# Optimization experiments

Measured on AMD Instinct MI355X. Metric: run time of the kernel, lower is better.

Reference implementation:

```python
import jax, jax.numpy as jnp
import numpy as np

B, T, E, H, D = 4, 2048, 1024, 16, 64


def setup_inputs() -> dict:
    key = jax.random.key(0)
    k1, k2, k3, k4 = jax.random.split(key, 4)
    s = 1.0 / np.sqrt(E)
    return {
        "x": jax.random.normal(k1, (B, T, E), dtype=jnp.float32),
        "wj_w": jax.random.uniform(k2, (E, E), jnp.float32, -s, s),   # torch Linear weight (out,in)
        "wjv_w": jax.random.uniform(k3, (E, E), jnp.float32, -s, s),
        "wo_w": jax.random.uniform(k4, (E, H * D), jnp.float32, -s, s),
    }


def reference(x, wj_w, wjv_w, wo_w):
    b, t, e = x.shape
    # echo = x @ wj_w.T ; eb = echo @ wj_w  (F.linear with transposed weight)
    eb = (x @ wj_w.T) @ wj_w
    sc = jnp.sum(x * eb, axis=-1) / jnp.sqrt(jnp.asarray(e, x.dtype))  # (B,T)
    # rank-1 outer-product scores with strict-upper causal mask
    ja = sc[:, :, None] * sc[:, None, :]                               # (B,T,T)
    causal = jnp.tril(jnp.ones((t, t), dtype=bool))
    ja = jnp.where(causal[None], ja, -jnp.inf)
    ja = jax.nn.softmax(ja, axis=-1)                                   # (B,T,T)
    # values per head; attention map shared across heads (broadcast, not materialized)
    val = (x @ wjv_w.T).reshape(b, t, H, D)                            # (B,T,H,D)
    out = jnp.einsum("bts,bshd->bthd", ja, val)                       # (B,T,H,D)
    return out.reshape(b, t, H * D) @ wo_w.T                           # (B,T,E)
```

## Files before the change

kernel.cpp:

```cpp
#include <hip/hip_runtime.h>
#include <math.h>

#define R_ROWS 8192
#define T_SEQ  2048
#define E_DIM  1024
#define KC     32

typedef __attribute__((ext_vector_type(8))) short short8;
typedef __attribute__((ext_vector_type(4))) float f32x4;

__device__ __forceinline__ ushort f2bf(float f) {
  uint u = __float_as_uint(f);
  u += 0x7FFFu + ((u >> 16) & 1u);
  return (ushort)(u >> 16);
}
__device__ __forceinline__ float bf2f(ushort h) {
  return __uint_as_float(((uint)h) << 16);
}


__global__ __launch_bounds__(256) void cvt_split_frag(
    const float* __restrict__ in, ushort* __restrict__ hi,
    ushort* __restrict__ lo, int n)
{
  int g = blockIdx.x * 256 + threadIdx.x;
  if (g >= n) return;
  const int l = g & 15, h = (g >> 4) & 3;
  const int pq = g >> 6;
  const int q = pq & (KC - 1), p = pq >> 5;
  const size_t src = (size_t)(p * 16 + l) * 1024 + q * 32 + h * 8;
  const float4 v0 = *(const float4*)&in[src];
  const float4 v1 = *(const float4*)&in[src + 4];
  ushort hh[8], ll[8];
  const float v[8] = {v0.x, v0.y, v0.z, v0.w, v1.x, v1.y, v1.z, v1.w};
#pragma unroll
  for (int e = 0; e < 8; ++e) {
    hh[e] = f2bf(v[e]);
    ll[e] = f2bf(v[e] - bf2f(hh[e]));
  }
  *(uint4*)&hi[(size_t)g * 8] = *(const uint4*)hh;
  *(uint4*)&lo[(size_t)g * 8] = *(const uint4*)ll;
}

__global__ __launch_bounds__(256) void cvt_bf16_frag(
    const float* __restrict__ in, ushort* __restrict__ out, int n)
{
  int g = blockIdx.x * 256 + threadIdx.x;
  if (g >= n) return;
  const int l = g & 15, h = (g >> 4) & 3;
  const int pq = g >> 6;
  const int q = pq & (KC - 1), p = pq >> 5;
  const size_t src = (size_t)(p * 16 + l) * 1024 + q * 32 + h * 8;
  const float4 v0 = *(const float4*)&in[src];
  const float4 v1 = *(const float4*)&in[src + 4];
  ushort hh[8];
  const float v[8] = {v0.x, v0.y, v0.z, v0.w, v1.x, v1.y, v1.z, v1.w};
#pragma unroll
  for (int e = 0; e < 8; ++e) hh[e] = f2bf(v[e]);
  *(uint4*)&out[(size_t)g * 8] = *(const uint4*)hh;
}

__global__ __launch_bounds__(256) void cvt_bf16(
    const float* __restrict__ in, ushort* __restrict__ out, int n4)
{
  int i = blockIdx.x * 256 + threadIdx.x;
  if (i >= n4) return;
  float4 v = ((const float4*)in)[i];
  ushort4 o;
  o.x = f2bf(v.x); o.y = f2bf(v.y); o.z = f2bf(v.z); o.w = f2bf(v.w);
  ((ushort4*)out)[i] = o;
}

struct Frags { short8 ah[4], al[4], bh[4], bl[4]; };

__global__ __launch_bounds__(256, 2) void gemm_sq_direct(
    const ushort* __restrict__ xh, const ushort* __restrict__ xl,
    const ushort* __restrict__ wh, const ushort* __restrict__ wl,
    float* __restrict__ sc_raw)
{
  const int tid = threadIdx.x;
  const int m0 = blockIdx.y * 128, n0 = blockIdx.x * 128;
  const int wave = tid >> 6, lane = tid & 63;
  const int l15 = lane & 15, lq = lane >> 4;
  const int wm = (wave & 1) * 64, wn = (wave >> 1) * 64;

  size_t aoff[4], boff[4];
#pragma unroll
  for (int i = 0; i < 4; ++i)
    aoff[i] = ((size_t)(((m0 + wm) >> 4) + i) * KC * 4 + lq) * 128 + l15 * 8;
#pragma unroll
  for (int j = 0; j < 4; ++j)
    boff[j] = ((size_t)(((n0 + wn) >> 4) + j) * KC * 4 + lq) * 128 + l15 * 8;

  f32x4 acc[4][4] = {};
  Frags f0, f1;

  auto load = [&](Frags& f, int q) {
    const size_t dq = (size_t)q * 512;
#pragma unroll
    for (int i = 0; i < 4; ++i) {
      f.ah[i] = *(const short8*)(xh + aoff[i] + dq);
      f.al[i] = *(const short8*)(xl + aoff[i] + dq);
    }
#pragma unroll
    for (int j = 0; j < 4; ++j) {
      f.bh[j] = *(const short8*)(wh + boff[j] + dq);
      f.bl[j] = *(const short8*)(wl + boff[j] + dq);
    }
  };
  auto step = [&](const Frags& f) {
#pragma unroll
    for (int i = 0; i < 4; ++i)
#pragma unroll
      for (int j = 0; j < 4; ++j) {
        acc[i][j] = __builtin_amdgcn_mfma_f32_16x16x32_bf16(f.ah[i], f.bh[j], acc[i][j], 0, 0, 0);
        acc[i][j] = __builtin_amdgcn_mfma_f32_16x16x32_bf16(f.ah[i], f.bl[j], acc[i][j], 0, 0, 0);
        acc[i][j] = __builtin_amdgcn_mfma_f32_16x16x32_bf16(f.al[i], f.bh[j], acc[i][j], 0, 0, 0);
      }
  };

  load(f0, 0);
#pragma unroll 1
  for (int q = 0; q < KC; q += 2) {
    load(f1, q + 1);
    step(f0);
    if (q + 2 < KC) load(f0, q + 2);
    step(f1);
  }

  __shared__ float red[128][33];
#pragma unroll
  for (int i = 0; i < 4; ++i)
#pragma unroll
    for (int r = 0; r < 4; ++r) {
      const int row = wm + i * 16 + lq * 4 + r;
      float s = 0.f;
#pragma unroll
      for (int j = 0; j < 4; ++j) s += acc[i][j][r] * acc[i][j][r];
      red[row][(l15 << 1) | (wave >> 1)] = s;
    }
  __syncthreads();
  if (tid < 128) {
    float s = 0.f;
#pragma unroll
    for (int c = 0; c < 32; ++c) s += red[tid][c];
    atomicAdd(&sc_raw[m0 + tid], s);
  }
}

__global__ __launch_bounds__(1024) void scan_max(
    const float* __restrict__ sc_raw, float* __restrict__ sc,
    float* __restrict__ pmax)
{
  const int b = blockIdx.x;
  __shared__ float b0[T_SEQ];
  __shared__ float b1[T_SEQ];
  const int tid = threadIdx.x;
  for (int i = tid; i < T_SEQ; i += 1024) {
    const float v = sc_raw[b*T_SEQ + i] * 0.03125f;
    b0[i] = v;
    sc[b*T_SEQ + i] = v;
  }
  __syncthreads();
  float* src = b0; float* dst = b1;
  for (int off = 1; off < T_SEQ; off <<= 1) {
    for (int i = tid; i < T_SEQ; i += 1024)
      dst[i] = (i >= off) ? fmaxf(src[i], src[i - off]) : src[i];
    __syncthreads();
    float* tmp = src; src = dst; dst = tmp;
  }
  for (int i = tid; i < T_SEQ; i += 1024) pmax[b*T_SEQ + i] = src[i];
}

template<bool OUT_BF16>
__global__ __launch_bounds__(256) void gemm_bf16_bfrag(
    const ushort* __restrict__ A, const ushort* __restrict__ Bf,
    void* __restrict__ Cout, int N, int K)
{
  __shared__ ushort As[128][40];
  const int tid = threadIdx.x;
  const int m0 = blockIdx.y * 128, n0 = blockIdx.x * 128;
  const int wave = tid >> 6, lane = tid & 63;
  const int l15 = lane & 15, lq = lane >> 4;
  const int wm = (wave & 1) * 64, wn = (wave >> 1) * 64;
  const int srow = tid >> 2, scol = (tid & 3) * 8;
  const int Kc = K >> 5;

  f32x4 acc[4][4] = {};
  const ushort* Ap = A + (size_t)(m0 + srow) * K + scol;
  size_t boff[4];
#pragma unroll
  for (int j = 0; j < 4; ++j)
    boff[j] = ((size_t)(((n0 + wn) >> 4) + j) * Kc * 4 + lq) * 128 + l15 * 8;

  for (int q = 0; q < Kc; ++q) {
    const uint4 a0 = *(const uint4*)(Ap + q * 32);
    const uint4 a1 = *(const uint4*)(Ap + (size_t)64 * K + q * 32);
    short8 bfr[4];
#pragma unroll
    for (int j = 0; j < 4; ++j)
      bfr[j] = *(const short8*)(Bf + boff[j] + (size_t)q * 512);
    __syncthreads();
    *(uint4*)&As[srow     ][scol] = a0;
    *(uint4*)&As[srow + 64][scol] = a1;
    __syncthreads();
    short8 af[4];
#pragma unroll
    for (int i = 0; i < 4; ++i)
      af[i] = *(const short8*)&As[wm + i*16 + l15][lq*8];
#pragma unroll
    for (int i = 0; i < 4; ++i)
#pragma unroll
      for (int j = 0; j < 4; ++j)
        acc[i][j] = __builtin_amdgcn_mfma_f32_16x16x32_bf16(af[i], bfr[j], acc[i][j], 0, 0, 0);
  }

#pragma unroll
  for (int i = 0; i < 4; ++i)
#pragma unroll
    for (int j = 0; j < 4; ++j) {
      const int mb = m0 + wm + i*16 + lq*4;
      const int nb = n0 + wn + j*16 + l15;
#pragma unroll
      for (int r = 0; r < 4; ++r) {
        if (OUT_BF16)
          ((ushort*)Cout)[(size_t)(mb + r) * N + nb] = f2bf(acc[i][j][r]);
        else
          ((float*)Cout)[(size_t)(mb + r) * N + nb] = acc[i][j][r];
      }
    }
}

__global__ __launch_bounds__(512) void attn_mfma(
    const ushort* __restrict__ valT, const float* __restrict__ sc,
    const float* __restrict__ pmax, ushort* __restrict__ attnN)
{
  __shared__ float scs_all[T_SEQ];
  __shared__ ushort p[2][128][72];
  __shared__ float zsh[128][4];
  __shared__ float zinv[128];

  const int b  = blockIdx.z;
  const int e0 = blockIdx.x * 128;
  const int tid = threadIdx.x;
  const int wave = tid >> 6, lane = tid & 63;
  const int l15 = lane & 15, lq = lane >> 4;
  const int wm = (wave & 1) * 64;
  const int wn = (wave >> 1) * 32;
  const int bT = b * T_SEQ;

  *(float4*)&scs_all[tid * 4] = *(const float4*)&sc[bT + tid * 4];
  __syncthreads();

  const int prow = tid >> 2;
  const int pc = (tid & 3) * 16;

#pragma unroll 1
  for (int ph = 0; ph < 2; ++ph) {
    const int ty = ph == 0 ? (15 - (int)blockIdx.y) : (int)blockIdx.y;
    const int t0 = ty * 128;
    const int nchunk = 2 * ty + 2;

    const int tglob = t0 + prow;
    const float st = sc[bT + tglob];
    const float pm = pmax[bT + tglob];

    f32x4 acc[4][2] = {};
    float zp = 0.f;

    auto pgen = [&](int c, int buf) -> float {
      const int s0 = c * 64;
      float sv[16];
#pragma unroll
      for (int q = 0; q < 4; ++q)
        *(float4*)&sv[q*4] = *(const float4*)&scs_all[s0 + pc + q*4];
      ushort tmp[16];
      float z = 0.f;
#pragma unroll
      for (int k = 0; k < 16; ++k) {
        const int sg = s0 + pc + k;
        float pe = 0.f;
        if (sg <= tglob) pe = __expf(st * (sv[k] - pm));
        const ushort h = f2bf(pe);
        tmp[k] = h;
        z += bf2f(h);
      }
      *(uint4*)&p[buf][prow][pc    ] = *(const uint4*)&tmp[0];
      *(uint4*)&p[buf][prow][pc + 8] = *(const uint4*)&tmp[8];
      return z;
    };

    auto loadB = [&](short8* dst, int c) {
#pragma unroll
      for (int j = 0; j < 2; ++j)
#pragma unroll
        for (int ksi = 0; ksi < 2; ++ksi)
          dst[j*2 + ksi] = *(const short8*)&valT[
              (size_t)(e0 + wn + j*16 + l15) * R_ROWS + bT + c*64 + ksi*32 + lq*8];
    };

    auto mstep = [&](int buf, const short8* bfr) {
#pragma unroll
      for (int ksi = 0; ksi < 2; ++ksi) {
        short8 af[4];
#pragma unroll
        for (int i = 0; i < 4; ++i)
          af[i] = *(const short8*)&p[buf][wm + i*16 + l15][ksi*32 + lq*8];
#pragma unroll
        for (int i = 0; i < 4; ++i)
#pragma unroll
          for (int j = 0; j < 2; ++j)
            acc[i][j] = __builtin_amdgcn_mfma_f32_16x16x32_bf16(
                af[i], bfr[j*2 + ksi], acc[i][j], 0, 0, 0);
      }
    };

    short8 bA[4], bB[4];
    zp += pgen(0, 0);
    loadB(bA, 0);
    __syncthreads();

#pragma unroll 1
    for (int c = 0; c < nchunk; ++c) {
      if ((c & 1) == 0) {
        if (c + 1 < nchunk) { loadB(bB, c + 1); zp += pgen(c + 1, 1); }
        mstep(0, bA);
      } else {
        if (c + 1 < nchunk) { loadB(bA, c + 1); zp += pgen(c + 1, 0); }
        mstep(1, bB);
      }
      __syncthreads();
    }

    zsh[prow][tid & 3] = zp;
    __syncthreads();
    if (tid < 128)
      zinv[tid] = 1.0f / (zsh[tid][0] + zsh[tid][1] + zsh[tid][2] + zsh[tid][3]);
    __syncthreads();

#pragma unroll
    for (int i = 0; i < 4; ++i)
#pragma unroll
      for (int j = 0; j < 2; ++j) {
        const int nb = e0 + wn + j*16 + l15;
#pragma unroll
        for (int r = 0; r < 4; ++r) {
          const int ml = wm + i*16 + lq*4 + r;
          const float v = acc[i][j][r] * zinv[ml];
          attnN[(size_t)(bT + t0 + ml) * E_DIM + nb] = f2bf(v);
        }
      }
    __syncthreads();
  }
}

extern "C" void kernel_launch(void* const* d_in, const int* in_sizes, int n_in,
                              void* d_out, int out_size, void* d_ws, size_t ws_size,
                              hipStream_t stream) {
  (void)in_sizes; (void)n_in; (void)out_size; (void)ws_size;
  const float* x   = (const float*)d_in[0];
  const float* wj  = (const float*)d_in[1];
  const float* wjv = (const float*)d_in[2];
  const float* wo  = (const float*)d_in[3];
  float* out = (float*)d_out;

  ushort* xh_f  = (ushort*)d_ws;
  ushort* xl_f  = xh_f  + (size_t)R_ROWS * E_DIM;
  ushort* wjh_f = xl_f  + (size_t)R_ROWS * E_DIM;
  ushort* wjl_f = wjh_f + (size_t)E_DIM * E_DIM;
  ushort* wjvb  = wjl_f + (size_t)E_DIM * E_DIM;
  ushort* wob_f = wjvb  + (size_t)E_DIM * E_DIM;
  float* sc_raw = (float*)(wob_f + (size_t)E_DIM * E_DIM);
  float* sc     = sc_raw + R_ROWS;
  float* pmax   = sc + R_ROWS;
  ushort* valT  = xl_f;
  ushort* attnN = xh_f;

  hipMemsetAsync(sc_raw, 0, R_ROWS * sizeof(float), stream);

  cvt_split_frag<<<R_ROWS*E_DIM/8/256, 256, 0, stream>>>(x,  xh_f,  xl_f,  R_ROWS*E_DIM/8);
  cvt_split_frag<<<E_DIM*E_DIM/8/256, 256, 0, stream>>>(wj, wjh_f, wjl_f, E_DIM*E_DIM/8);
  cvt_bf16<<<E_DIM*E_DIM/4/256, 256, 0, stream>>>(wjv, wjvb, E_DIM*E_DIM/4);
  cvt_bf16_frag<<<E_DIM*E_DIM/8/256, 256, 0, stream>>>(wo, wob_f, E_DIM*E_DIM/8);

  gemm_sq_direct<<<dim3(E_DIM/128, R_ROWS/128), 256, 0, stream>>>(
      xh_f, xl_f, wjh_f, wjl_f, sc_raw);
  scan_max<<<4, 1024, 0, stream>>>(sc_raw, sc, pmax);

  gemm_bf16_bfrag<true><<<dim3(R_ROWS/128, E_DIM/128), 256, 0, stream>>>(
      wjvb, xh_f, valT, R_ROWS, E_DIM);

  attn_mfma<<<dim3(E_DIM/128, 8, 4), 512, 0, stream>>>(valT, sc, pmax, attnN);

  gemm_bf16_bfrag<false><<<dim3(E_DIM/128, R_ROWS/128), 256, 0, stream>>>(
      attnN, wob_f, out, E_DIM, E_DIM);
}
```

Baseline: 276.6 us.

## Fold output projection into value weights via precomputed Wo·Wjv product

Uses associativity to precompute M = Wo·Wjv (1024x1024, split-bf16 precision) so the value GEMM directly yields projected values. The attention kernel then writes the final fp32 output, which removes the last 8192x1024x1024 GEMM and the attnN round trip. It adds a small weight-product GEMM plus transposed split conversion. Softmax normalization now sums unrounded probabilities, which slightly changes rounding.

```diff
diff --git a/kernel.cpp b/kernel.cpp
--- a/kernel.cpp
+++ b/kernel.cpp
@@ -42,33 +42,26 @@
   *(uint4*)&lo[(size_t)g * 8] = *(const uint4*)ll;
 }
 
-__global__ __launch_bounds__(256) void cvt_bf16_frag(
-    const float* __restrict__ in, ushort* __restrict__ out, int n)
+__global__ __launch_bounds__(256) void cvt_splitT_frag(
+    const float* __restrict__ in, ushort* __restrict__ hi,
+    ushort* __restrict__ lo, int n)
 {
   int g = blockIdx.x * 256 + threadIdx.x;
   if (g >= n) return;
   const int l = g & 15, h = (g >> 4) & 3;
   const int pq = g >> 6;
   const int q = pq & (KC - 1), p = pq >> 5;
-  const size_t src = (size_t)(p * 16 + l) * 1024 + q * 32 + h * 8;
-  const float4 v0 = *(const float4*)&in[src];
-  const float4 v1 = *(const float4*)&in[src + 4];
-  ushort hh[8];
-  const float v[8] = {v0.x, v0.y, v0.z, v0.w, v1.x, v1.y, v1.z, v1.w};
-#pragma unroll
-  for (int e = 0; e < 8; ++e) hh[e] = f2bf(v[e]);
-  *(uint4*)&out[(size_t)g * 8] = *(const uint4*)hh;
-}
-
-__global__ __launch_bounds__(256) void cvt_bf16(
-    const float* __restrict__ in, ushort* __restrict__ out, int n4)
-{
-  int i = blockIdx.x * 256 + threadIdx.x;
-  if (i >= n4) return;
-  float4 v = ((const float4*)in)[i];
-  ushort4 o;
-  o.x = f2bf(v.x); o.y = f2bf(v.y); o.z = f2bf(v.z); o.w = f2bf(v.w);
-  ((ushort4*)out)[i] = o;
+  const int rr = p * 16 + l;
+  const int cc = q * 32 + h * 8;
+  ushort hh[8], ll[8];
+#pragma unroll
+  for (int e = 0; e < 8; ++e) {
+    const float v = in[(size_t)(cc + e) * 1024 + rr];
+    hh[e] = f2bf(v);
+    ll[e] = f2bf(v - bf2f(hh[e]));
+  }
+  *(uint4*)&hi[(size_t)g * 8] = *(const uint4*)hh;
+  *(uint4*)&lo[(size_t)g * 8] = *(const uint4*)ll;
 }
 
 struct Frags { short8 ah[4], al[4], bh[4], bl[4]; };
@@ -146,6 +139,73 @@
     for (int c = 0; c < 32; ++c) s += red[tid][c];
     atomicAdd(&sc_raw[m0 + tid], s);
   }
+}
+
+__global__ __launch_bounds__(256, 2) void gemm_m_split(
+    const ushort* __restrict__ ah_, const ushort* __restrict__ al_,
+    const ushort* __restrict__ bh_, const ushort* __restrict__ bl_,
+    ushort* __restrict__ Mh)
+{
+  const int tid = threadIdx.x;
+  const int m0 = blockIdx.y * 128, n0 = blockIdx.x * 128;
+  const int wave = tid >> 6, lane = tid & 63;
+  const int l15 = lane & 15, lq = lane >> 4;
+  const int wm = (wave & 1) * 64, wn = (wave >> 1) * 64;
+
+  size_t aoff[4], boff[4];
+#pragma unroll
+  for (int i = 0; i < 4; ++i)
+    aoff[i] = ((size_t)(((m0 + wm) >> 4) + i) * KC * 4 + lq) * 128 + l15 * 8;
+#pragma unroll
+  for (int j = 0; j < 4; ++j)
+    boff[j] = ((size_t)(((n0 + wn) >> 4) + j) * KC * 4 + lq) * 128 + l15 * 8;
+
+  f32x4 acc[4][4] = {};
+  Frags f0, f1;
+
+  auto load = [&](Frags& f, int q) {
+    const size_t dq = (size_t)q * 512;
+#pragma unroll
+    for (int i = 0; i < 4; ++i) {
+      f.ah[i] = *(const short8*)(ah_ + aoff[i] + dq);
+      f.al[i] = *(const short8*)(al_ + aoff[i] + dq);
+    }
+#pragma unroll
+    for (int j = 0; j < 4; ++j) {
+      f.bh[j] = *(const short8*)(bh_ + boff[j] + dq);
+      f.bl[j] = *(const short8*)(bl_ + boff[j] + dq);
+    }
+  };
+  auto step = [&](const Frags& f) {
+#pragma unroll
+    for (int i = 0; i < 4; ++i)
+#pragma unroll
+      for (int j = 0; j < 4; ++j) {
+        acc[i][j] = __builtin_amdgcn_mfma_f32_16x16x32_bf16(f.ah[i], f.bh[j], acc[i][j], 0, 0, 0);
+        acc[i][j] = __builtin_amdgcn_mfma_f32_16x16x32_bf16(f.ah[i], f.bl[j], acc[i][j], 0, 0, 0);
+        acc[i][j] = __builtin_amdgcn_mfma_f32_16x16x32_bf16(f.al[i], f.bh[j], acc[i][j], 0, 0, 0);
+      }
+  };
+
+  load(f0, 0);
+#pragma unroll 1
+  for (int q = 0; q < KC; q += 2) {
+    load(f1, q + 1);
+    step(f0);
+    if (q + 2 < KC) load(f0, q + 2);
+    step(f1);
+  }
+
+#pragma unroll
+  for (int i = 0; i < 4; ++i)
+#pragma unroll
+    for (int j = 0; j < 4; ++j) {
+      const int mb = m0 + wm + i * 16 + lq * 4;
+      const int nb = n0 + wn + j * 16 + l15;
+#pragma unroll
+      for (int r = 0; r < 4; ++r)
+        Mh[(size_t)(mb + r) * E_DIM + nb] = f2bf(acc[i][j][r]);
+    }
 }
 
 __global__ __launch_bounds__(1024) void scan_max(
@@ -233,7 +293,7 @@
 
 __global__ __launch_bounds__(512) void attn_mfma(
     const ushort* __restrict__ valT, const float* __restrict__ sc,
-    const float* __restrict__ pmax, ushort* __restrict__ attnN)
+    const float* __restrict__ pmax, float* __restrict__ outp)
 {
   __shared__ float scs_all[T_SEQ];
   __shared__ ushort p[2][128][72];
@@ -281,9 +341,8 @@
         const int sg = s0 + pc + k;
         float pe = 0.f;
         if (sg <= tglob) pe = __expf(st * (sv[k] - pm));
-        const ushort h = f2bf(pe);
-        tmp[k] = h;
-        z += bf2f(h);
+        tmp[k] = f2bf(pe);
+        z += pe;
       }
       *(uint4*)&p[buf][prow][pc    ] = *(const uint4*)&tmp[0];
       *(uint4*)&p[buf][prow][pc + 8] = *(const uint4*)&tmp[8];
@@ -346,8 +405,7 @@
 #pragma unroll
         for (int r = 0; r < 4; ++r) {
           const int ml = wm + i*16 + lq*4 + r;
-          const float v = acc[i][j][r] * zinv[ml];
-          attnN[(size_t)(bT + t0 + ml) * E_DIM + nb] = f2bf(v);
+          outp[(size_t)(bT + t0 + ml) * E_DIM + nb] = acc[i][j][r] * zinv[ml];
         }
       }
     __syncthreads();
@@ -366,32 +424,31 @@
 
   ushort* xh_f  = (ushort*)d_ws;
   ushort* xl_f  = xh_f  + (size_t)R_ROWS * E_DIM;
-  ushort* wjh_f = xl_f  + (size_t)R_ROWS * E_DIM;
-  ushort* wjl_f = wjh_f + (size_t)E_DIM * E_DIM;
-  ushort* wjvb  = wjl_f + (size_t)E_DIM * E_DIM;
-  ushort* wob_f = wjvb  + (size_t)E_DIM * E_DIM;
-  float* sc_raw = (float*)(wob_f + (size_t)E_DIM * E_DIM);
+  ushort* bufA  = xl_f  + (size_t)R_ROWS * E_DIM;
+  ushort* bufB  = bufA  + (size_t)E_DIM * E_DIM;
+  ushort* bufC  = bufB  + (size_t)E_DIM * E_DIM;
+  ushort* bufD  = bufC  + (size_t)E_DIM * E_DIM;
+  ushort* Mh    = bufD  + (size_t)E_DIM * E_DIM;
+  float* sc_raw = (float*)(Mh + (size_t)E_DIM * E_DIM);
   float* sc     = sc_raw + R_ROWS;
   float* pmax   = sc + R_ROWS;
-  ushort* valT  = xl_f;
-  ushort* attnN = xh_f;
+  ushort* WT    = xl_f;
 
   hipMemsetAsync(sc_raw, 0, R_ROWS * sizeof(float), stream);
 
-  cvt_split_frag<<<R_ROWS*E_DIM/8/256, 256, 0, stream>>>(x,  xh_f,  xl_f,  R_ROWS*E_DIM/8);
-  cvt_split_frag<<<E_DIM*E_DIM/8/256, 256, 0, stream>>>(wj, wjh_f, wjl_f, E_DIM*E_DIM/8);
-  cvt_bf16<<<E_DIM*E_DIM/4/256, 256, 0, stream>>>(wjv, wjvb, E_DIM*E_DIM/4);
-  cvt_bf16_frag<<<E_DIM*E_DIM/8/256, 256, 0, stream>>>(wo, wob_f, E_DIM*E_DIM/8);
+  cvt_split_frag <<<E_DIM*E_DIM/8/256, 256, 0, stream>>>(wo,  bufA, bufB, E_DIM*E_DIM/8);
+  cvt_splitT_frag<<<E_DIM*E_DIM/8/256, 256, 0, stream>>>(wjv, bufC, bufD, E_DIM*E_DIM/8);
+  gemm_m_split<<<dim3(E_DIM/128, E_DIM/128), 256, 0, stream>>>(bufA, bufB, bufC, bufD, Mh);
+
+  cvt_split_frag<<<R_ROWS*E_DIM/8/256, 256, 0, stream>>>(x,  xh_f, xl_f, R_ROWS*E_DIM/8);
+  cvt_split_frag<<<E_DIM*E_DIM/8/256, 256, 0, stream>>>(wj, bufA, bufB, E_DIM*E_DIM/8);
 
   gemm_sq_direct<<<dim3(E_DIM/128, R_ROWS/128), 256, 0, stream>>>(
-      xh_f, xl_f, wjh_f, wjl_f, sc_raw);
+      xh_f, xl_f, bufA, bufB, sc_raw);
   scan_max<<<4, 1024, 0, stream>>>(sc_raw, sc, pmax);
 
   gemm_bf16_bfrag<true><<<dim3(R_ROWS/128, E_DIM/128), 256, 0, stream>>>(
-      wjvb, xh_f, valT, R_ROWS, E_DIM);
-
-  attn_mfma<<<dim3(E_DIM/128, 8, 4), 512, 0, stream>>>(valT, sc, pmax, attnN);
-
-  gemm_bf16_bfrag<false><<<dim3(E_DIM/128, R_ROWS/128), 256, 0, stream>>>(
-      attnN, wob_f, out, E_DIM, E_DIM);
-}
+      Mh, xh_f, WT, R_ROWS, E_DIM);
+
+  attn_mfma<<<dim3(E_DIM/128, 8, 4), 512, 0, stream>>>(WT, sc, pmax, out);
+}
```

Measured after the change: 281.3 us. About the same (+1.7%).
